# Kernel tuning notes

Hardware: AMD Instinct MI355X
Metric: run time of the kernel (lower is better)

Reference implementation:

```python
import jax, jax.numpy as jnp
import numpy as np

N_NODES = 50000
N_EDGES = 800000
ND = 10      # node feature dim
ED = 10      # edge feature dim
H = 128      # hidden dim
C = 2        # num classes
BN_EPS = 1e-5


def setup_inputs() -> dict:
    key = jax.random.key(0)
    ks = jax.random.split(key, 32)

    def glorot(i, shape):
        fan_in, fan_out = shape[-2], shape[-1]
        s = np.sqrt(6.0 / (fan_in + fan_out))
        return jax.random.uniform(ks[i], shape, dtype=jnp.float32, minval=-s, maxval=s)

    inp = {
        "x": jax.random.normal(ks[0], (N_NODES, ND), dtype=jnp.float32),
        "edge_index": jax.random.randint(ks[1], (2, N_EDGES), 0, N_NODES),
        "edge_attr": jax.random.normal(ks[2], (N_EDGES, ED), dtype=jnp.float32),
        # node encoder: Linear(ND,H), ReLU, Dropout, Linear(H,H)
        "ne_w1": glorot(3, (ND, H)), "ne_b1": jnp.zeros((H,), jnp.float32),
        "ne_w2": glorot(4, (H, H)),  "ne_b2": jnp.zeros((H,), jnp.float32),
        # edge encoder: Linear(ED,H), ReLU, Dropout, Linear(H,H)
        "ee_w1": glorot(5, (ED, H)), "ee_b1": jnp.zeros((H,), jnp.float32),
        "ee_w2": glorot(6, (H, H)),  "ee_b2": jnp.zeros((H,), jnp.float32),
        # edge attention: Linear(2H+ED,H), ReLU, Linear(H,1), Sigmoid
        "ea_w1": glorot(7, (2 * H + ED, H)), "ea_b1": jnp.zeros((H,), jnp.float32),
        "ea_w2": glorot(8, (H, 1)),          "ea_b2": jnp.zeros((1,), jnp.float32),
        # 3 GCN layers (weight + bias), 3 batchnorms, 2 skip linears
        "gcn_w": glorot(9, (3, H, H)),  "gcn_b": jnp.zeros((3, H), jnp.float32),
        "bn_g": jnp.ones((3, H), jnp.float32), "bn_b": jnp.zeros((3, H), jnp.float32),
        "skip_w": glorot(10, (2, H, H)), "skip_b": jnp.zeros((2, H), jnp.float32),
        # classifier: Linear(2H,H), ReLU, Linear(H,H//2), ReLU, Linear(H//2,C)
        "cl_w1": glorot(11, (2 * H, H)),   "cl_b1": jnp.zeros((H,), jnp.float32),
        "cl_w2": glorot(12, (H, H // 2)),  "cl_b2": jnp.zeros((H // 2,), jnp.float32),
        "cl_w3": glorot(13, (H // 2, C)),  "cl_b3": jnp.zeros((C,), jnp.float32),
    }
    return inp


def reference(x, edge_index, edge_attr,
              ne_w1, ne_b1, ne_w2, ne_b2,
              ee_w1, ee_b1, ee_w2, ee_b2,
              ea_w1, ea_b1, ea_w2, ea_b2,
              gcn_w, gcn_b, bn_g, bn_b, skip_w, skip_b,
              cl_w1, cl_b1, cl_w2, cl_b2, cl_w3, cl_b3):
    n = x.shape[0]
    row, col = edge_index[0], edge_index[1]

    # node encoder (dropout is identity in eval)
    h = jax.nn.relu(x @ ne_w1 + ne_b1) @ ne_w2 + ne_b2

    # GCN normalization with self-loops (PyG GCNConv, symmetric norm)
    sl = jnp.arange(n)
    row_f = jnp.concatenate([row, sl])   # source
    col_f = jnp.concatenate([col, sl])   # target
    deg = jax.ops.segment_sum(jnp.ones_like(row_f, dtype=h.dtype), col_f, num_segments=n)
    dinv = jnp.where(deg > 0, jax.lax.rsqrt(jnp.maximum(deg, 1.0)) * (deg > 0), 0.0)
    dinv = jnp.where(deg > 0, deg ** -0.5, 0.0)
    norm = (dinv[row_f] * dinv[col_f])[:, None]  # [E+N, 1]

    for i in range(3):
        h_prev = h
        m = h @ gcn_w[i]                                            # transform
        h = jax.ops.segment_sum(norm * m[row_f], col_f, num_segments=n) + gcn_b[i]
        # batchnorm (batch statistics over nodes)
        mu = h.mean(axis=0)
        var = h.var(axis=0)
        h = (h - mu) / jnp.sqrt(var + BN_EPS) * bn_g[i] + bn_b[i]
        h = jax.nn.relu(h)
        if i > 0:
            h = h + h_prev @ skip_w[i - 1] + skip_b[i - 1]

    # edge-level head
    h_r = h[row]            # [E, H]
    h_c = h[col]            # [E, H]
    edge_repr = jnp.concatenate([h_r, h_c], axis=1)                 # [E, 2H]
    edge_feat = jax.nn.relu(edge_attr @ ee_w1 + ee_b1) @ ee_w2 + ee_b2
    att_in = jnp.concatenate([h_r, h_c, edge_attr], axis=1)         # [E, 2H+ED]
    att = jax.nn.sigmoid(jax.nn.relu(att_in @ ea_w1 + ea_b1) @ ea_w2 + ea_b2)  # [E,1]
    w_ef = att * edge_feat
    edge_repr = edge_repr + jnp.concatenate([w_ef, w_ef], axis=1)

    # classifier MLP
    z = jax.nn.relu(edge_repr @ cl_w1 + cl_b1)
    z = jax.nn.relu(z @ cl_w2 + cl_b2)
    logits = z @ cl_w3 + cl_b3                                       # [E, C]
    return logits
```

## Files before the change

kernel.cpp:

```cpp
#include <hip/hip_runtime.h>
#include <math.h>

#define NN 50000
#define NE 800000
#define H 128

typedef short bf16x8 __attribute__((ext_vector_type(8)));
typedef unsigned short u16x8 __attribute__((ext_vector_type(8)));
typedef float f32x4 __attribute__((ext_vector_type(4)));
typedef unsigned short u16;

__device__ inline u16 f2b(float f) {
  unsigned u = __float_as_uint(f);
  return (u16)((u + 0x7FFF + ((u >> 16) & 1)) >> 16);
}
__device__ inline float b2f(u16 s) { return __uint_as_float(((unsigned)s) << 16); }

__global__ void k_prep(const float* __restrict__ ea_w1, const float* __restrict__ cl_w1,
                       const float* __restrict__ ee_w2, const float* __restrict__ cl_w2,
                       const float* __restrict__ gcn_w, const float* __restrict__ skip_w,
                       const float* __restrict__ ne_w2, const float* __restrict__ ee_w1,
                       u16* __restrict__ WP) {
  int idx = blockIdx.x * 256 + threadIdx.x;
  if (idx >= 212992) return;
  float v;
  if (idx < 16384) {
    int n = idx >> 7, k = idx & 127;
    v = ne_w2[k * 128 + n];
  } else if (idx < 65536) {
    int lo = idx - 16384; int i = lo >> 14; int n = (lo >> 7) & 127, k = lo & 127;
    v = gcn_w[i * 16384 + k * 128 + n];
  } else if (idx < 98304) {
    int lo = idx - 65536; int i = lo >> 14; int n = (lo >> 7) & 127, k = lo & 127;
    v = skip_w[i * 16384 + k * 128 + n];
  } else if (idx < 163840) {
    int lo = idx - 98304; int tab = lo >> 14; int n = (lo >> 7) & 127, k = lo & 127;
    if (tab == 0) v = ea_w1[k * 128 + n];
    else if (tab == 1) v = cl_w1[k * 128 + n];
    else if (tab == 2) v = ea_w1[(128 + k) * 128 + n];
    else v = cl_w1[(128 + k) * 128 + n];
  } else if (idx < 180224) {
    int lo = idx - 163840; int n = lo >> 7, k = lo & 127;
    v = cl_w1[k * 128 + n] + cl_w1[(128 + k) * 128 + n];
  } else if (idx < 196608) {
    int lo = idx - 180224; int n = lo >> 7, k = lo & 127;
    v = ee_w2[k * 128 + n];
  } else if (idx < 204800) {
    int lo = idx - 196608; int n = lo >> 7, k = lo & 127;
    v = cl_w2[k * 64 + n];
  } else if (idx < 208896) {
    int lo = idx - 204800; int n = lo >> 5, k = lo & 31;
    v = (k < 10) ? ee_w1[k * 128 + n] : 0.f;
  } else {
    int lo = idx - 208896; int n = lo >> 5, k = lo & 31;
    v = (k < 10) ? ea_w1[(256 + k) * 128 + n] : 0.f;
  }
  WP[idx] = f2b(v);
}

__global__ __launch_bounds__(256) void k_rowenc(
    const float* __restrict__ x, const float* __restrict__ w1,
    const float* __restrict__ b1, u16* __restrict__ t1) {
  __shared__ float xs[16][10];
  int t = threadIdx.x;
  int base = blockIdx.x * 16;
  for (int idx = t; idx < 160; idx += 256) xs[idx / 10][idx % 10] = x[base * 10 + idx];
  __syncthreads();
  int j = t & 127, eg = t >> 7;
  float acc[8];
#pragma unroll
  for (int i = 0; i < 8; ++i) acc[i] = b1[j];
  for (int k = 0; k < 10; ++k) {
    float w = w1[k * H + j];
#pragma unroll
    for (int i = 0; i < 8; ++i) acc[i] += xs[eg * 8 + i][k] * w;
  }
#pragma unroll
  for (int i = 0; i < 8; ++i) t1[(long)(base + eg * 8 + i) * H + j] = f2b(fmaxf(acc[i], 0.f));
}


__global__ __launch_bounds__(256, 2) void k_ngemm(
    const u16* __restrict__ A, const u16* __restrict__ WT,
    const float* __restrict__ bias, u16* __restrict__ outB) {
  __shared__ u16 As[128 * 128];
  int t = threadIdx.x;
  long base = (long)blockIdx.x * 128;
  for (int idx = t; idx < 128 * 16; idx += 256) {
    int row = idx >> 4, k8 = (idx & 15) * 8;
    long gr = base + row; if (gr >= NN) gr = 0;
    uint4 v = *(const uint4*)(A + gr * 128 + k8);
    *(uint4*)(As + row * 128 + (k8 ^ ((row & 7) * 8))) = v;
  }
  __syncthreads();
  int l = t & 63, w = t >> 6;
  int wrow = w * 32;
  int cl_ = l & 15, gr = l >> 4, ko = gr * 8;
  f32x4 acc[2][8];
#pragma unroll
  for (int nt = 0; nt < 8; ++nt) {
    float bb = bias[nt * 16 + cl_];
#pragma unroll
    for (int mt = 0; mt < 2; ++mt) { acc[mt][nt][0] = bb; acc[mt][nt][1] = bb; acc[mt][nt][2] = bb; acc[mt][nt][3] = bb; }
  }
#pragma unroll
  for (int c = 0; c < 4; ++c) {
    bf16x8 a[2], b[8];
#pragma unroll
    for (int mt = 0; mt < 2; ++mt) {
      int row = wrow + mt * 16 + cl_;
      a[mt] = *(const bf16x8*)(As + row * 128 + ((c * 32 + ko) ^ ((row & 7) * 8)));
    }
#pragma unroll
    for (int nt = 0; nt < 8; ++nt)
      b[nt] = *(const bf16x8*)(WT + (nt * 16 + cl_) * 128 + c * 32 + ko);
#pragma unroll
    for (int mt = 0; mt < 2; ++mt)
#pragma unroll
      for (int nt = 0; nt < 8; ++nt)
        acc[mt][nt] = __builtin_amdgcn_mfma_f32_16x16x32_bf16(a[mt], b[nt], acc[mt][nt], 0, 0, 0);
  }
#pragma unroll
  for (int mt = 0; mt < 2; ++mt)
#pragma unroll
    for (int r = 0; r < 4; ++r) {
      long row = base + wrow + mt * 16 + gr * 4 + r;
      if (row >= NN) continue;
#pragma unroll
      for (int nt = 0; nt < 8; ++nt)
        outB[row * 128 + nt * 16 + cl_] = f2b(acc[mt][nt][r]);
    }
}

__global__ __launch_bounds__(256, 2) void k_gcnskip(
    const u16* __restrict__ Ain, const u16* __restrict__ WTg, const u16* __restrict__ WTs,
    const float* __restrict__ dinv, u16* __restrict__ mn, float* __restrict__ Af) {
  __shared__ u16 As[128 * 128];
  int t = threadIdx.x;
  long base = (long)blockIdx.x * 128;
  for (int idx = t; idx < 128 * 16; idx += 256) {
    int row = idx >> 4, k8 = (idx & 15) * 8;
    long gr = base + row; if (gr >= NN) gr = 0;
    uint4 v = *(const uint4*)(Ain + gr * 128 + k8);
    *(uint4*)(As + row * 128 + (k8 ^ ((row & 7) * 8))) = v;
  }
  __syncthreads();
  const u16* WT = blockIdx.y ? WTs : WTg;
  int l = t & 63, w = t >> 6;
  int wrow = w * 32;
  int cl_ = l & 15, gr = l >> 4, ko = gr * 8;
  f32x4 acc[2][8];
#pragma unroll
  for (int nt = 0; nt < 8; ++nt)
#pragma unroll
    for (int mt = 0; mt < 2; ++mt) { acc[mt][nt][0] = 0.f; acc[mt][nt][1] = 0.f; acc[mt][nt][2] = 0.f; acc[mt][nt][3] = 0.f; }
#pragma unroll
  for (int c = 0; c < 4; ++c) {
    bf16x8 a[2], b[8];
#pragma unroll
    for (int mt = 0; mt < 2; ++mt) {
      int row = wrow + mt * 16 + cl_;
      a[mt] = *(const bf16x8*)(As + row * 128 + ((c * 32 + ko) ^ ((row & 7) * 8)));
    }
#pragma unroll
    for (int nt = 0; nt < 8; ++nt)
      b[nt] = *(const bf16x8*)(WT + (nt * 16 + cl_) * 128 + c * 32 + ko);
#pragma unroll
    for (int mt = 0; mt < 2; ++mt)
#pragma unroll
      for (int nt = 0; nt < 8; ++nt)
        acc[mt][nt] = __builtin_amdgcn_mfma_f32_16x16x32_bf16(a[mt], b[nt], acc[mt][nt], 0, 0, 0);
  }
  bool isG = (blockIdx.y == 0);
#pragma unroll
  for (int mt = 0; mt < 2; ++mt)
#pragma unroll
    for (int r = 0; r < 4; ++r) {
      long row = base + wrow + mt * 16 + gr * 4 + r;
      if (row >= NN) continue;
      float dv = isG ? dinv[row] : 0.f;
#pragma unroll
      for (int nt = 0; nt < 8; ++nt) {
        int col = nt * 16 + cl_;
        if (isG) mn[row * 128 + col] = f2b(dv * acc[mt][nt][r]);
        else Af[row * 128 + col] = acc[mt][nt][r];
      }
    }
}

__global__ __launch_bounds__(256, 2) void k_ntab(
    const u16* __restrict__ A, const u16* __restrict__ WPt4,
    const float* __restrict__ ea_b1, const float* __restrict__ cl_b1,
    u16* __restrict__ T1, u16* __restrict__ T2) {
  __shared__ u16 As[128 * 128];
  int t = threadIdx.x;
  long base = (long)blockIdx.x * 128;
  for (int idx = t; idx < 128 * 16; idx += 256) {
    int row = idx >> 4, k8 = (idx & 15) * 8;
    long gr = base + row; if (gr >= NN) gr = 0;
    uint4 v = *(const uint4*)(A + gr * 128 + k8);
    *(uint4*)(As + row * 128 + (k8 ^ ((row & 7) * 8))) = v;
  }
  __syncthreads();
  int y = blockIdx.y;
  const u16* WT = WPt4 + y * 16384;
  const float* bias = (y == 0) ? ea_b1 : ((y == 1) ? cl_b1 : nullptr);
  u16* outT = (y < 2) ? T1 : T2;
  int colOff = (y & 1) * 128;
  int l = t & 63, w = t >> 6;
  int wrow = w * 32;
  int cl_ = l & 15, gr = l >> 4, ko = gr * 8;
  f32x4 acc[2][8];
#pragma unroll
  for (int nt = 0; nt < 8; ++nt) {
    float bb = bias ? bias[nt * 16 + cl_] : 0.f;
#pragma unroll
    for (int mt = 0; mt < 2; ++mt) { acc[mt][nt][0] = bb; acc[mt][nt][1] = bb; acc[mt][nt][2] = bb; acc[mt][nt][3] = bb; }
  }
#pragma unroll
  for (int c = 0; c < 4; ++c) {
    bf16x8 a[2], b[8];
#pragma unroll
    for (int mt = 0; mt < 2; ++mt) {
      int row = wrow + mt * 16 + cl_;
      a[mt] = *(const bf16x8*)(As + row * 128 + ((c * 32 + ko) ^ ((row & 7) * 8)));
    }
#pragma unroll
    for (int nt = 0; nt < 8; ++nt)
      b[nt] = *(const bf16x8*)(WT + (nt * 16 + cl_) * 128 + c * 32 + ko);
#pragma unroll
    for (int mt = 0; mt < 2; ++mt)
#pragma unroll
      for (int nt = 0; nt < 8; ++nt)
        acc[mt][nt] = __builtin_amdgcn_mfma_f32_16x16x32_bf16(a[mt], b[nt], acc[mt][nt], 0, 0, 0);
  }
#pragma unroll
  for (int mt = 0; mt < 2; ++mt)
#pragma unroll
    for (int r = 0; r < 4; ++r) {
      long row = base + wrow + mt * 16 + gr * 4 + r;
      if (row >= NN) continue;
#pragma unroll
      for (int nt = 0; nt < 8; ++nt)
        outT[row * 256 + colOff + nt * 16 + cl_] = f2b(acc[mt][nt][r]);
    }
}

__global__ void k_deg(const int* __restrict__ col, unsigned* __restrict__ deg) {
  int e = blockIdx.x * 256 + threadIdx.x;
  if (e < NE) atomicAdd(&deg[col[e]], 1u);
}

__global__ __launch_bounds__(256) void k_scan1(const unsigned* __restrict__ deg,
                                               int* __restrict__ bsum) {
  __shared__ int s[256];
  int t = threadIdx.x, v = blockIdx.x * 256 + t;
  s[t] = (v < NN) ? (int)deg[v] : 0;
  __syncthreads();
  for (int off = 128; off > 0; off >>= 1) {
    if (t < off) s[t] += s[t + off];
    __syncthreads();
  }
  if (t == 0) bsum[blockIdx.x] = s[0];
}
__global__ __launch_bounds__(256) void k_scan2(const int* __restrict__ bsum,
                                               int* __restrict__ boff, int nb) {
  __shared__ int s[256];
  int t = threadIdx.x;
  int v = (t < nb) ? bsum[t] : 0;
  s[t] = v;
  __syncthreads();
  for (int off = 1; off < 256; off <<= 1) {
    int x = (t >= off) ? s[t - off] : 0;
    __syncthreads();
    s[t] += x;
    __syncthreads();
  }
  if (t < nb) boff[t] = s[t] - v;
}
__global__ __launch_bounds__(256) void k_scan3(const unsigned* __restrict__ deg,
                                               const int* __restrict__ boff,
                                               int* __restrict__ offs, int* __restrict__ cursor,
                                               float* __restrict__ dinv) {
  __shared__ int s[256];
  int t = threadIdx.x, v = blockIdx.x * 256 + t;
  int d = (v < NN) ? (int)deg[v] : 0;
  s[t] = d;
  __syncthreads();
  for (int off = 1; off < 256; off <<= 1) {
    int x = (t >= off) ? s[t - off] : 0;
    __syncthreads();
    s[t] += x;
    __syncthreads();
  }
  int excl = s[t] - d + boff[blockIdx.x];
  if (v < NN) {
    offs[v] = excl; cursor[v] = excl;
    dinv[v] = 1.0f / sqrtf((float)(d + 1));
  }
}
__global__ void k_fill(const int* __restrict__ ei, int* __restrict__ cursor,
                       int* __restrict__ elr, int* __restrict__ ecn, int* __restrict__ eid) {
  int e = blockIdx.x * 256 + threadIdx.x;
  if (e < NE) {
    int c = ei[NE + e];
    int pos = atomicAdd(&cursor[c], 1);
    elr[pos] = ei[e];
    ecn[pos] = c;
    eid[pos] = e;
  }
}

__global__ __launch_bounds__(256) void k_agg(
    const int* __restrict__ offs, const unsigned* __restrict__ deg,
    const int* __restrict__ elr, const float* __restrict__ dinv,
    const u16* __restrict__ mn, const float* __restrict__ gb,
    float* __restrict__ agg, double* __restrict__ sums) {
  __shared__ float s_lds[16][128];
  __shared__ float q_lds[16][128];
  int t = threadIdx.x;
  int slot = t >> 4;
  int j8 = (t & 15) * 8;
  float ps[8], pq[8];
#pragma unroll
  for (int k = 0; k < 8; ++k) { ps[k] = 0.f; pq[k] = 0.f; }
  int vbase = blockIdx.x * 64;
  for (int nn = 0; nn < 4; ++nn) {
    int v = vbase + nn * 16 + slot;
    if (v < NN) {
      float acc[8];
      u16x8 m0 = *(const u16x8*)(mn + (long)v * 128 + j8);
#pragma unroll
      for (int k = 0; k < 8; ++k) acc[k] = b2f(m0[k]);
      int start = offs[v];
      int cnt = (int)deg[v];
      for (int i = 0; i < cnt; ++i) {
        u16x8 m = *(const u16x8*)(mn + (long)elr[start + i] * 128 + j8);
#pragma unroll
        for (int k = 0; k < 8; ++k) acc[k] += b2f(m[k]);
      }
      float dv = dinv[v];
#pragma unroll
      for (int k = 0; k < 8; ++k) {
        acc[k] = dv * acc[k] + gb[j8 + k];
        ps[k] += acc[k];
        pq[k] += acc[k] * acc[k];
      }
      *(float4*)(agg + (long)v * 128 + j8) = make_float4(acc[0], acc[1], acc[2], acc[3]);
      *(float4*)(agg + (long)v * 128 + j8 + 4) = make_float4(acc[4], acc[5], acc[6], acc[7]);
    }
  }
#pragma unroll
  for (int k = 0; k < 8; ++k) { s_lds[slot][j8 + k] = ps[k]; q_lds[slot][j8 + k] = pq[k]; }
  __syncthreads();
  if (t < 128) {
    float s = 0.f;
#pragma unroll
    for (int sl = 0; sl < 16; ++sl) s += s_lds[sl][t];
    atomicAdd(&sums[t], (double)s);
  } else {
    int j = t - 128;
    float q = 0.f;
#pragma unroll
    for (int sl = 0; sl < 16; ++sl) q += q_lds[sl][j];
    atomicAdd(&sums[128 + j], (double)q);
  }
}

template <bool SKIP>
__global__ __launch_bounds__(256) void k_bnskip(
    const float* __restrict__ agg, const double* __restrict__ sums,
    const float* __restrict__ g, const float* __restrict__ b,
    const float* __restrict__ skipv, const float* __restrict__ skipb,
    u16* __restrict__ hb) {
  int idx = blockIdx.x * 256 + threadIdx.x;
  int j = idx & 127;
  double mu = sums[j] * (1.0 / NN);
  double var = sums[128 + j] * (1.0 / NN) - mu * mu;
  float inv = (float)(1.0 / sqrt(var + 1e-5));
  float val = (float)((double)agg[idx] - mu) * inv * g[j] + b[j];
  val = fmaxf(val, 0.f);
  if (SKIP) val += skipv[idx] + skipb[j];
  hb[idx] = f2b(val);
}

#define EPB 128
__global__ __launch_bounds__(256, 2) void k_edge(
    const int* __restrict__ elr, const int* __restrict__ ecn, const int* __restrict__ eid,
    const float* __restrict__ eaf,
    const u16* __restrict__ T1, const u16* __restrict__ T2,
    const float* __restrict__ ee_b1, const float* __restrict__ ee_b2,
    const float* __restrict__ ea_w2, const float* __restrict__ ea_b2,
    const u16* __restrict__ WT_ee1, const u16* __restrict__ WT_eae,
    const u16* __restrict__ WT_ee2, const u16* __restrict__ WT_ab,
    const u16* __restrict__ WT_cl2,
    const float* __restrict__ cl_b2, const float* __restrict__ cl_w3,
    const float* __restrict__ cl_b3,
    float* __restrict__ out) {
  __shared__ u16 ebuf[128 * 128];
  __shared__ u16 ustage[8192];
  __shared__ float attP[256];
  __shared__ float attS[128];

  int t = threadIdx.x;
  long ebase = (long)blockIdx.x * EPB;
  int e = t & 127, half = t >> 7;
  int jb0 = half * 64;
  int rn = elr[ebase + e];
  int cn = ecn[ebase + e];

  int l = t & 63, w = t >> 6;
  int wrow = w * 32;
  int cl_ = l & 15, g4 = l >> 4, ko = g4 * 8;

  int srow = wrow + (l >> 1);
  int cq = (l & 1) * 32;
  int rs = elr[ebase + srow];
  int cs = ecn[ebase + srow];
  u16* cstage = ustage + w * 2048;

  u16x8 h1p[8];
#pragma unroll
  for (int k = 0; k < 8; ++k)
    h1p[k] = *(const u16x8*)(T1 + (long)rn * 256 + jb0 + k * 8);
  u16x8 v1p[8];
#pragma unroll
  for (int k = 0; k < 8; ++k) {
    int hh = k >> 2, kk = k & 3;
    v1p[k] = *(const u16x8*)(T1 + (long)rs * 256 + 128 + hh * 64 + cq + kk * 8);
  }

  {
    int k0 = half * 16;
    long ge = eid[ebase + e];
    const float* src = eaf + ge * 10;
#pragma unroll
    for (int k = 0; k < 16; ++k) {
      int kk = k0 + k;
      ustage[e * 32 + kk] = (kk < 10) ? f2b(src[kk]) : (u16)0;
    }
  }
  __syncthreads();

  {
    bf16x8 aEA[2];
#pragma unroll
    for (int mt = 0; mt < 2; ++mt)
      aEA[mt] = *(const bf16x8*)(ustage + (wrow + mt * 16 + cl_) * 32 + ko);
    bf16x8 b[8];
#pragma unroll
    for (int nt = 0; nt < 8; ++nt)
      b[nt] = *(const bf16x8*)(WT_eae + (nt * 16 + cl_) * 32 + ko);
#pragma unroll
    for (int mt = 0; mt < 2; ++mt)
#pragma unroll
      for (int nt = 0; nt < 8; ++nt) {
        f32x4 pa = {0.f, 0.f, 0.f, 0.f};
        pa = __builtin_amdgcn_mfma_f32_16x16x32_bf16(aEA[mt], b[nt], pa, 0, 0, 0);
#pragma unroll
        for (int r = 0; r < 4; ++r) {
          int row = wrow + mt * 16 + g4 * 4 + r;
          int col = nt * 16 + cl_;
          ebuf[row * 128 + (col ^ ((row & 7) * 8))] = f2b(pa[r]);
        }
      }
  }
  __syncthreads();

  {
    float s = 0.f;
#pragma unroll
    for (int k = 0; k < 8; ++k) {
      int jb = jb0 + k * 8;
      u16x8 h1 = h1p[k];
      u16x8 h2 = *(const u16x8*)(T2 + (long)cn * 256 + jb);
      u16x8 pp = *(const u16x8*)(ebuf + e * 128 + (jb ^ ((e & 7) * 8)));
#pragma unroll
      for (int i = 0; i < 8; ++i)
        s += fmaxf(b2f(h1[i]) + b2f(h2[i]) + b2f(pp[i]), 0.f) * ea_w2[jb + i];
    }
    attP[half * 128 + e] = s;
  }
  __syncthreads();

  if (t < 128) attS[t] = 1.f / (1.f + __expf(-(attP[t] + attP[128 + t] + ea_b2[0])));

  {
    bf16x8 aEA[2];
#pragma unroll
    for (int mt = 0; mt < 2; ++mt)
      aEA[mt] = *(const bf16x8*)(ustage + (wrow + mt * 16 + cl_) * 32 + ko);
    bf16x8 b[8];
#pragma unroll
    for (int nt = 0; nt < 8; ++nt)
      b[nt] = *(const bf16x8*)(WT_ee1 + (nt * 16 + cl_) * 32 + ko);
#pragma unroll
    for (int mt = 0; mt < 2; ++mt)
#pragma unroll
      for (int nt = 0; nt < 8; ++nt) {
        float bb = ee_b1[nt * 16 + cl_];
        f32x4 ua;
        ua[0] = bb; ua[1] = bb; ua[2] = bb; ua[3] = bb;
        ua = __builtin_amdgcn_mfma_f32_16x16x32_bf16(aEA[mt], b[nt], ua, 0, 0, 0);
#pragma unroll
        for (int r = 0; r < 4; ++r) {
          int row = wrow + mt * 16 + g4 * 4 + r;
          int col = nt * 16 + cl_;
          ebuf[row * 128 + (col ^ ((row & 7) * 8))] = f2b(fmaxf(ua[r], 0.f));
        }
      }
  }
  __syncthreads();

  {
    bf16x8 a2[4][2];
#pragma unroll
    for (int c = 0; c < 4; ++c)
#pragma unroll
      for (int mt = 0; mt < 2; ++mt) {
        int row = wrow + mt * 16 + cl_;
        a2[c][mt] = *(const bf16x8*)(ebuf + row * 128 + ((c * 32 + ko) ^ ((row & 7) * 8)));
      }
#pragma unroll
    for (int hh = 0; hh < 2; ++hh) {
      f32x4 acc[2][4];
#pragma unroll
      for (int n4 = 0; n4 < 4; ++n4) {
        float bb = ee_b2[(hh * 4 + n4) * 16 + cl_];
#pragma unroll
        for (int mt = 0; mt < 2; ++mt) { acc[mt][n4][0] = bb; acc[mt][n4][1] = bb; acc[mt][n4][2] = bb; acc[mt][n4][3] = bb; }
      }
#pragma unroll
      for (int c = 0; c < 4; ++c)
#pragma unroll
        for (int n4 = 0; n4 < 4; ++n4) {
          bf16x8 b = *(const bf16x8*)(WT_ee2 + ((hh * 4 + n4) * 16 + cl_) * 128 + c * 32 + ko);
#pragma unroll
          for (int mt = 0; mt < 2; ++mt)
            acc[mt][n4] = __builtin_amdgcn_mfma_f32_16x16x32_bf16(a2[c][mt], b, acc[mt][n4], 0, 0, 0);
        }
#pragma unroll
      for (int mt = 0; mt < 2; ++mt)
#pragma unroll
        for (int r = 0; r < 4; ++r) {
          int row = wrow + mt * 16 + g4 * 4 + r;
          float av = attS[row];
#pragma unroll
          for (int n4 = 0; n4 < 4; ++n4) {
            int col = (hh * 4 + n4) * 16 + cl_;
            ebuf[row * 128 + (col ^ ((row & 7) * 8))] = f2b(av * acc[mt][n4][r]);
          }
        }
    }
  }

  {
    bf16x8 a2[4][2];
#pragma unroll
    for (int c = 0; c < 4; ++c)
#pragma unroll
      for (int mt = 0; mt < 2; ++mt) {
        int row = wrow + mt * 16 + cl_;
        a2[c][mt] = *(const bf16x8*)(ebuf + row * 128 + ((c * 32 + ko) ^ ((row & 7) * 8)));
      }
#pragma unroll
    for (int hh = 0; hh < 2; ++hh) {
      f32x4 acc[2][4];
#pragma unroll
      for (int n4 = 0; n4 < 4; ++n4)
#pragma unroll
        for (int mt = 0; mt < 2; ++mt) { acc[mt][n4][0] = 0.f; acc[mt][n4][1] = 0.f; acc[mt][n4][2] = 0.f; acc[mt][n4][3] = 0.f; }
#pragma unroll
      for (int c = 0; c < 4; ++c)
#pragma unroll
        for (int n4 = 0; n4 < 4; ++n4) {
          bf16x8 b = *(const bf16x8*)(WT_ab + ((hh * 4 + n4) * 16 + cl_) * 128 + c * 32 + ko);
#pragma unroll
          for (int mt = 0; mt < 2; ++mt)
            acc[mt][n4] = __builtin_amdgcn_mfma_f32_16x16x32_bf16(a2[c][mt], b, acc[mt][n4], 0, 0, 0);
        }
      u16x8 v2[4];
#pragma unroll
      for (int k = 0; k < 4; ++k)
        v2[k] = *(const u16x8*)(T2 + (long)cs * 256 + 128 + hh * 64 + cq + k * 8);
#pragma unroll
      for (int k = 0; k < 4; ++k) {
        u16x8 p;
#pragma unroll
        for (int i = 0; i < 8; ++i) p[i] = f2b(b2f(v1p[hh * 4 + k][i]) + b2f(v2[k][i]));
        *(u16x8*)(cstage + (srow & 31) * 64 + ((cq + k * 8) ^ ((srow & 7) * 8))) = p;
      }
#pragma unroll
      for (int mt = 0; mt < 2; ++mt)
#pragma unroll
        for (int r = 0; r < 4; ++r) {
          int row = wrow + mt * 16 + g4 * 4 + r;
#pragma unroll
          for (int n4 = 0; n4 < 4; ++n4) {
            int col = (hh * 4 + n4) * 16 + cl_;
            int cc = col - hh * 64;
            float v = acc[mt][n4][r] + b2f(cstage[(row & 31) * 64 + (cc ^ ((row & 7) * 8))]);
            ebuf[row * 128 + (col ^ ((row & 7) * 8))] = f2b(fmaxf(v, 0.f));
          }
        }
    }
  }

  f32x4 acc2[2][4];
#pragma unroll
  for (int nt = 0; nt < 4; ++nt) {
    float bb = cl_b2[nt * 16 + cl_];
#pragma unroll
    for (int mt = 0; mt < 2; ++mt) { acc2[mt][nt][0] = bb; acc2[mt][nt][1] = bb; acc2[mt][nt][2] = bb; acc2[mt][nt][3] = bb; }
  }
#pragma unroll
  for (int c = 0; c < 4; ++c) {
    bf16x8 a[2], b[4];
#pragma unroll
    for (int mt = 0; mt < 2; ++mt) {
      int row = wrow + mt * 16 + cl_;
      a[mt] = *(const bf16x8*)(ebuf + row * 128 + ((c * 32 + ko) ^ ((row & 7) * 8)));
    }
#pragma unroll
    for (int nt = 0; nt < 4; ++nt)
      b[nt] = *(const bf16x8*)(WT_cl2 + (nt * 16 + cl_) * 128 + c * 32 + ko);
#pragma unroll
    for (int mt = 0; mt < 2; ++mt)
#pragma unroll
      for (int nt = 0; nt < 4; ++nt)
        acc2[mt][nt] = __builtin_amdgcn_mfma_f32_16x16x32_bf16(a[mt], b[nt], acc2[mt][nt], 0, 0, 0);
  }
#pragma unroll
  for (int mt = 0; mt < 2; ++mt)
#pragma unroll
    for (int r = 0; r < 4; ++r) {
      int row = wrow + mt * 16 + g4 * 4 + r;
#pragma unroll
      for (int nt = 0; nt < 4; ++nt) {
        int col = nt * 16 + cl_;
        ebuf[row * 128 + (col ^ ((row & 7) * 8))] = f2b(fmaxf(acc2[mt][nt][r], 0.f));
      }
    }
  __syncthreads();

  if (t < 128) {
    long ge = eid[ebase + t];
    float o0 = cl_b3[0], o1 = cl_b3[1];
    for (int k8 = 0; k8 < 64; k8 += 8) {
      u16x8 v = *(const u16x8*)(ebuf + t * 128 + (k8 ^ ((t & 7) * 8)));
#pragma unroll
      for (int i = 0; i < 8; ++i) {
        float z = b2f(v[i]);
        o0 += z * cl_w3[(k8 + i) * 2];
        o1 += z * cl_w3[(k8 + i) * 2 + 1];
      }
    }
    *(float2*)(out + ge * 2) = make_float2(o0, o1);
  }
}

extern "C" void kernel_launch(void* const* d_in, const int* in_sizes, int n_in,
                              void* d_out, int out_size, void* d_ws, size_t ws_size,
                              hipStream_t stream) {
  (void)in_sizes; (void)n_in; (void)out_size; (void)ws_size;
  const float* x = (const float*)d_in[0];
  const int* ei = (const int*)d_in[1];
  const float* eattr = (const float*)d_in[2];
  const float* ne_w1 = (const float*)d_in[3];
  const float* ne_b1 = (const float*)d_in[4];
  const float* ne_w2 = (const float*)d_in[5];
  const float* ne_b2 = (const float*)d_in[6];
  const float* ee_w1 = (const float*)d_in[7];
  const float* ee_b1 = (const float*)d_in[8];
  const float* ee_w2 = (const float*)d_in[9];
  const float* ee_b2 = (const float*)d_in[10];
  const float* ea_w1 = (const float*)d_in[11];
  const float* ea_b1 = (const float*)d_in[12];
  const float* ea_w2 = (const float*)d_in[13];
  const float* ea_b2 = (const float*)d_in[14];
  const float* gcn_w = (const float*)d_in[15];
  const float* gcn_b = (const float*)d_in[16];
  const float* bn_g = (const float*)d_in[17];
  const float* bn_b = (const float*)d_in[18];
  const float* skip_w = (const float*)d_in[19];
  const float* skip_b = (const float*)d_in[20];
  const float* cl_w1 = (const float*)d_in[21];
  const float* cl_b1 = (const float*)d_in[22];
  const float* cl_w2 = (const float*)d_in[23];
  const float* cl_b2 = (const float*)d_in[24];
  const float* cl_w3 = (const float*)d_in[25];
  const float* cl_b3 = (const float*)d_in[26];
  float* out = (float*)d_out;

  char* ws = (char*)d_ws;
  u16* hb0 = (u16*)ws;
  u16* hb1 = (u16*)(ws + 12800000);
  float* A = (float*)(ws + 25600000);
  u16* mn = (u16*)(ws + 51200000);
  float* agg = (float*)(ws + 64000000);
  unsigned* deg = (unsigned*)(ws + 89600000);
  float* dinv = (float*)(ws + 89800000);
  double* sums = (double*)(ws + 90000000);
  u16* WP = (u16*)(ws + 90002048);
  int* offs = (int*)(ws + 90428032);
  int* cursor = (int*)(ws + 90628032);
  int* bsum = (int*)(ws + 90828032);
  int* boff = (int*)(ws + 90829056);
  int* elr = (int*)(ws + 90830080);
  int* ecn = (int*)(ws + 94030080);
  int* eid = (int*)(ws + 97230080);
  u16* T1 = (u16*)A;
  u16* T2 = (u16*)agg;

  u16* WP_ne2 = WP;
  u16* WP_gcn = WP + 16384;
  u16* WP_skip = WP + 65536;
  u16* WP_t4 = WP + 98304;
  u16* WP_ab = WP + 163840;
  u16* WP_ee2 = WP + 180224;
  u16* WP_cl2 = WP + 196608;
  u16* WP_ee1 = WP + 204800;
  u16* WP_eae = WP + 208896;

  const int* col = ei + NE;
  const int NGB = (NN + 255) / 256;
  const int NGB128 = (NN + 127) / 128;

  k_prep<<<832, 256, 0, stream>>>(ea_w1, cl_w1, ee_w2, cl_w2, gcn_w, skip_w, ne_w2, ee_w1, WP);
  hipMemsetAsync(deg, 0, NN * sizeof(unsigned), stream);
  k_deg<<<(NE + 255) / 256, 256, 0, stream>>>(col, deg);
  k_scan1<<<NGB, 256, 0, stream>>>(deg, bsum);
  k_scan2<<<1, 256, 0, stream>>>(bsum, boff, NGB);
  k_scan3<<<NGB, 256, 0, stream>>>(deg, boff, offs, cursor, dinv);
  k_fill<<<(NE + 255) / 256, 256, 0, stream>>>(ei, cursor, elr, ecn, eid);

  k_rowenc<<<NN / 16, 256, 0, stream>>>(x, ne_w1, ne_b1, hb1);
  k_ngemm<<<NGB128, 256, 0, stream>>>(hb1, WP_ne2, ne_b2, hb0);

  u16* hin = hb0; u16* hout = hb1;
  for (int i = 0; i < 3; ++i) {
    if (i > 0)
      k_gcnskip<<<dim3(NGB128, 2), 256, 0, stream>>>(hin, WP_gcn + (long)i * 16384,
                                                     WP_skip + (long)(i - 1) * 16384, dinv, mn, A);
    else
      k_gcnskip<<<dim3(NGB128, 1), 256, 0, stream>>>(hin, WP_gcn, nullptr, dinv, mn, nullptr);
    hipMemsetAsync(sums, 0, 256 * sizeof(double), stream);
    k_agg<<<(NN + 63) / 64, 256, 0, stream>>>(offs, deg, elr, dinv, mn, gcn_b + i * H, agg, sums);
    if (i > 0)
      k_bnskip<true><<<NN * H / 256, 256, 0, stream>>>(
          agg, sums, bn_g + i * H, bn_b + i * H, A, skip_b + (i - 1) * H, hout);
    else
      k_bnskip<false><<<NN * H / 256, 256, 0, stream>>>(
          agg, sums, bn_g, bn_b, nullptr, nullptr, hout);
    u16* tmp = hin; hin = hout; hout = tmp;
  }

  k_ntab<<<dim3(NGB128, 4), 256, 0, stream>>>(hin, WP_t4, ea_b1, cl_b1, T1, T2);

  k_edge<<<NE / EPB, 256, 0, stream>>>(
      elr, ecn, eid, eattr, T1, T2, ee_b1, ee_b2, ea_w2, ea_b2,
      WP_ee1, WP_eae, WP_ee2, WP_ab, WP_cl2, cl_b2, cl_w3, cl_b3, out);
}
```

Baseline: 907.1 us.

## Fuse node encoder, merge per-node GEMM grids, defer edge table loads

Replaces the scalar first node-encoder layer and the separate second-layer GEMM with one kernel that does both layers on MFMA. The intermediate activation stays in shared memory and x is converted to padded bf16. The GCN/skip and node-table kernels now loop over their weight matrices within one block instead of using blockIdx.y, so the A tile is loaded from global once rather than per y-slice. The edge kernel no longer prefetches T1 rows into registers at the start, and loads them later where they are used. This should cut register pressure, but the loads are no longer hidden behind other work.

```diff
diff --git a/kernel.cpp b/kernel.cpp
--- a/kernel.cpp
+++ b/kernel.cpp
@@ -20,9 +20,9 @@
                        const float* __restrict__ ee_w2, const float* __restrict__ cl_w2,
                        const float* __restrict__ gcn_w, const float* __restrict__ skip_w,
                        const float* __restrict__ ne_w2, const float* __restrict__ ee_w1,
-                       u16* __restrict__ WP) {
+                       const float* __restrict__ ne_w1, u16* __restrict__ WP) {
   int idx = blockIdx.x * 256 + threadIdx.x;
-  if (idx >= 212992) return;
+  if (idx >= 217088) return;
   float v;
   if (idx < 16384) {
     int n = idx >> 7, k = idx & 127;
@@ -51,55 +51,61 @@
   } else if (idx < 208896) {
     int lo = idx - 204800; int n = lo >> 5, k = lo & 31;
     v = (k < 10) ? ee_w1[k * 128 + n] : 0.f;
-  } else {
+  } else if (idx < 212992) {
     int lo = idx - 208896; int n = lo >> 5, k = lo & 31;
     v = (k < 10) ? ea_w1[(256 + k) * 128 + n] : 0.f;
+  } else {
+    int lo = idx - 212992; int n = lo >> 5, k = lo & 31;
+    v = (k < 10) ? ne_w1[k * 128 + n] : 0.f;
   }
   WP[idx] = f2b(v);
 }
 
-__global__ __launch_bounds__(256) void k_rowenc(
-    const float* __restrict__ x, const float* __restrict__ w1,
-    const float* __restrict__ b1, u16* __restrict__ t1) {
-  __shared__ float xs[16][10];
-  int t = threadIdx.x;
-  int base = blockIdx.x * 16;
-  for (int idx = t; idx < 160; idx += 256) xs[idx / 10][idx % 10] = x[base * 10 + idx];
-  __syncthreads();
-  int j = t & 127, eg = t >> 7;
-  float acc[8];
-#pragma unroll
-  for (int i = 0; i < 8; ++i) acc[i] = b1[j];
-  for (int k = 0; k < 10; ++k) {
-    float w = w1[k * H + j];
-#pragma unroll
-    for (int i = 0; i < 8; ++i) acc[i] += xs[eg * 8 + i][k] * w;
-  }
-#pragma unroll
-  for (int i = 0; i < 8; ++i) t1[(long)(base + eg * 8 + i) * H + j] = f2b(fmaxf(acc[i], 0.f));
-}
-
-
-__global__ __launch_bounds__(256, 2) void k_ngemm(
-    const u16* __restrict__ A, const u16* __restrict__ WT,
-    const float* __restrict__ bias, u16* __restrict__ outB) {
+__global__ __launch_bounds__(256, 2) void k_nodeenc(
+    const float* __restrict__ x, const u16* __restrict__ WT1,
+    const u16* __restrict__ WT2, const float* __restrict__ b1,
+    const float* __restrict__ b2, u16* __restrict__ outB) {
+  __shared__ u16 XL[128 * 32];
   __shared__ u16 As[128 * 128];
   int t = threadIdx.x;
   long base = (long)blockIdx.x * 128;
-  for (int idx = t; idx < 128 * 16; idx += 256) {
-    int row = idx >> 4, k8 = (idx & 15) * 8;
+  for (int idx = t; idx < 128 * 32; idx += 256) {
+    int row = idx >> 5, kk = idx & 31;
     long gr = base + row; if (gr >= NN) gr = 0;
-    uint4 v = *(const uint4*)(A + gr * 128 + k8);
-    *(uint4*)(As + row * 128 + (k8 ^ ((row & 7) * 8))) = v;
+    XL[idx] = (kk < 10) ? f2b(x[gr * 10 + kk]) : (u16)0;
   }
   __syncthreads();
   int l = t & 63, w = t >> 6;
   int wrow = w * 32;
-  int cl_ = l & 15, gr = l >> 4, ko = gr * 8;
+  int cl_ = l & 15, g4 = l >> 4, ko = g4 * 8;
+  {
+    bf16x8 a[2], b[8];
+#pragma unroll
+    for (int mt = 0; mt < 2; ++mt)
+      a[mt] = *(const bf16x8*)(XL + (wrow + mt * 16 + cl_) * 32 + ko);
+#pragma unroll
+    for (int nt = 0; nt < 8; ++nt)
+      b[nt] = *(const bf16x8*)(WT1 + (nt * 16 + cl_) * 32 + ko);
+#pragma unroll
+    for (int mt = 0; mt < 2; ++mt)
+#pragma unroll
+      for (int nt = 0; nt < 8; ++nt) {
+        float bb = b1[nt * 16 + cl_];
+        f32x4 ua;
+        ua[0] = bb; ua[1] = bb; ua[2] = bb; ua[3] = bb;
+        ua = __builtin_amdgcn_mfma_f32_16x16x32_bf16(a[mt], b[nt], ua, 0, 0, 0);
+#pragma unroll
+        for (int r = 0; r < 4; ++r) {
+          int row = wrow + mt * 16 + g4 * 4 + r;
+          int col = nt * 16 + cl_;
+          As[row * 128 + (col ^ ((row & 7) * 8))] = f2b(fmaxf(ua[r], 0.f));
+        }
+      }
+  }
   f32x4 acc[2][8];
 #pragma unroll
   for (int nt = 0; nt < 8; ++nt) {
-    float bb = bias[nt * 16 + cl_];
+    float bb = b2[nt * 16 + cl_];
 #pragma unroll
     for (int mt = 0; mt < 2; ++mt) { acc[mt][nt][0] = bb; acc[mt][nt][1] = bb; acc[mt][nt][2] = bb; acc[mt][nt][3] = bb; }
   }
@@ -113,7 +119,7 @@
     }
 #pragma unroll
     for (int nt = 0; nt < 8; ++nt)
-      b[nt] = *(const bf16x8*)(WT + (nt * 16 + cl_) * 128 + c * 32 + ko);
+      b[nt] = *(const bf16x8*)(WT2 + (nt * 16 + cl_) * 128 + c * 32 + ko);
 #pragma unroll
     for (int mt = 0; mt < 2; ++mt)
 #pragma unroll
@@ -124,7 +130,7 @@
   for (int mt = 0; mt < 2; ++mt)
 #pragma unroll
     for (int r = 0; r < 4; ++r) {
-      long row = base + wrow + mt * 16 + gr * 4 + r;
+      long row = base + wrow + mt * 16 + g4 * 4 + r;
       if (row >= NN) continue;
 #pragma unroll
       for (int nt = 0; nt < 8; ++nt)
@@ -145,47 +151,78 @@
     *(uint4*)(As + row * 128 + (k8 ^ ((row & 7) * 8))) = v;
   }
   __syncthreads();
-  const u16* WT = blockIdx.y ? WTs : WTg;
   int l = t & 63, w = t >> 6;
   int wrow = w * 32;
-  int cl_ = l & 15, gr = l >> 4, ko = gr * 8;
-  f32x4 acc[2][8];
-#pragma unroll
-  for (int nt = 0; nt < 8; ++nt)
-#pragma unroll
-    for (int mt = 0; mt < 2; ++mt) { acc[mt][nt][0] = 0.f; acc[mt][nt][1] = 0.f; acc[mt][nt][2] = 0.f; acc[mt][nt][3] = 0.f; }
-#pragma unroll
-  for (int c = 0; c < 4; ++c) {
-    bf16x8 a[2], b[8];
-#pragma unroll
-    for (int mt = 0; mt < 2; ++mt) {
-      int row = wrow + mt * 16 + cl_;
-      a[mt] = *(const bf16x8*)(As + row * 128 + ((c * 32 + ko) ^ ((row & 7) * 8)));
-    }
+  int cl_ = l & 15, g4 = l >> 4, ko = g4 * 8;
+  {
+    f32x4 acc[2][8];
 #pragma unroll
     for (int nt = 0; nt < 8; ++nt)
-      b[nt] = *(const bf16x8*)(WT + (nt * 16 + cl_) * 128 + c * 32 + ko);
-#pragma unroll
-    for (int mt = 0; mt < 2; ++mt)
+#pragma unroll
+      for (int mt = 0; mt < 2; ++mt) { acc[mt][nt][0] = 0.f; acc[mt][nt][1] = 0.f; acc[mt][nt][2] = 0.f; acc[mt][nt][3] = 0.f; }
+#pragma unroll
+    for (int c = 0; c < 4; ++c) {
+      bf16x8 a[2], b[8];
+#pragma unroll
+      for (int mt = 0; mt < 2; ++mt) {
+        int row = wrow + mt * 16 + cl_;
+        a[mt] = *(const bf16x8*)(As + row * 128 + ((c * 32 + ko) ^ ((row & 7) * 8)));
+      }
 #pragma unroll
       for (int nt = 0; nt < 8; ++nt)
-        acc[mt][nt] = __builtin_amdgcn_mfma_f32_16x16x32_bf16(a[mt], b[nt], acc[mt][nt], 0, 0, 0);
-  }
-  bool isG = (blockIdx.y == 0);
-#pragma unroll
-  for (int mt = 0; mt < 2; ++mt)
-#pragma unroll
-    for (int r = 0; r < 4; ++r) {
-      long row = base + wrow + mt * 16 + gr * 4 + r;
-      if (row >= NN) continue;
-      float dv = isG ? dinv[row] : 0.f;
-#pragma unroll
-      for (int nt = 0; nt < 8; ++nt) {
-        int col = nt * 16 + cl_;
-        if (isG) mn[row * 128 + col] = f2b(dv * acc[mt][nt][r]);
-        else Af[row * 128 + col] = acc[mt][nt][r];
-      }
-    }
+        b[nt] = *(const bf16x8*)(WTg + (nt * 16 + cl_) * 128 + c * 32 + ko);
+#pragma unroll
+      for (int mt = 0; mt < 2; ++mt)
+#pragma unroll
+        for (int nt = 0; nt < 8; ++nt)
+          acc[mt][nt] = __builtin_amdgcn_mfma_f32_16x16x32_bf16(a[mt], b[nt], acc[mt][nt], 0, 0, 0);
+    }
+#pragma unroll
+    for (int mt = 0; mt < 2; ++mt)
+#pragma unroll
+      for (int r = 0; r < 4; ++r) {
+        long row = base + wrow + mt * 16 + g4 * 4 + r;
+        if (row >= NN) continue;
+        float dv = dinv[row];
+#pragma unroll
+        for (int nt = 0; nt < 8; ++nt)
+          mn[row * 128 + nt * 16 + cl_] = f2b(dv * acc[mt][nt][r]);
+      }
+  }
+  if (WTs) {
+    f32x4 acc[2][8];
+#pragma unroll
+    for (int nt = 0; nt < 8; ++nt)
+#pragma unroll
+      for (int mt = 0; mt < 2; ++mt) { acc[mt][nt][0] = 0.f; acc[mt][nt][1] = 0.f; acc[mt][nt][2] = 0.f; acc[mt][nt][3] = 0.f; }
+#pragma unroll
+    for (int c = 0; c < 4; ++c) {
+      bf16x8 a[2], b[8];
+#pragma unroll
+      for (int mt = 0; mt < 2; ++mt) {
+        int row = wrow + mt * 16 + cl_;
+        a[mt] = *(const bf16x8*)(As + row * 128 + ((c * 32 + ko) ^ ((row & 7) * 8)));
+      }
+#pragma unroll
+      for (int nt = 0; nt < 8; ++nt)
+        b[nt] = *(const bf16x8*)(WTs + (nt * 16 + cl_) * 128 + c * 32 + ko);
+#pragma unroll
+      for (int mt = 0; mt < 2; ++mt)
+#pragma unroll
+        for (int nt = 0; nt < 8; ++nt)
+          acc[mt][nt] = __builtin_amdgcn_mfma_f32_16x16x32_bf16(a[mt], b[nt], acc[mt][nt], 0, 0, 0);
+    }
+#pragma unroll
+    for (int mt = 0; mt < 2; ++mt)
+#pragma unroll
+      for (int r = 0; r < 4; ++r) {
+        long row = base + wrow + mt * 16 + g4 * 4 + r;
+        if (row >= NN) continue;
+#pragma unroll
+        for (int nt = 0; nt < 8; ++nt)
+          Af[row * 128 + nt * 16 + cl_] = acc[mt][nt][r];
+      }
+  }
 }
 
 __global__ __launch_bounds__(256, 2) void k_ntab(
@@ -202,48 +239,49 @@
     *(uint4*)(As + row * 128 + (k8 ^ ((row & 7) * 8))) = v;
   }
   __syncthreads();
-  int y = blockIdx.y;
-  const u16* WT = WPt4 + y * 16384;
-  const float* bias = (y == 0) ? ea_b1 : ((y == 1) ? cl_b1 : nullptr);
-  u16* outT = (y < 2) ? T1 : T2;
-  int colOff = (y & 1) * 128;
   int l = t & 63, w = t >> 6;
   int wrow = w * 32;
-  int cl_ = l & 15, gr = l >> 4, ko = gr * 8;
-  f32x4 acc[2][8];
-#pragma unroll
-  for (int nt = 0; nt < 8; ++nt) {
-    float bb = bias ? bias[nt * 16 + cl_] : 0.f;
-#pragma unroll
-    for (int mt = 0; mt < 2; ++mt) { acc[mt][nt][0] = bb; acc[mt][nt][1] = bb; acc[mt][nt][2] = bb; acc[mt][nt][3] = bb; }
-  }
-#pragma unroll
-  for (int c = 0; c < 4; ++c) {
-    bf16x8 a[2], b[8];
-#pragma unroll
-    for (int mt = 0; mt < 2; ++mt) {
-      int row = wrow + mt * 16 + cl_;
-      a[mt] = *(const bf16x8*)(As + row * 128 + ((c * 32 + ko) ^ ((row & 7) * 8)));
-    }
-#pragma unroll
-    for (int nt = 0; nt < 8; ++nt)
-      b[nt] = *(const bf16x8*)(WT + (nt * 16 + cl_) * 128 + c * 32 + ko);
-#pragma unroll
-    for (int mt = 0; mt < 2; ++mt)
+  int cl_ = l & 15, g4 = l >> 4, ko = g4 * 8;
+  for (int y = 0; y < 4; ++y) {
+    const u16* WT = WPt4 + y * 16384;
+    const float* bias = (y == 0) ? ea_b1 : ((y == 1) ? cl_b1 : nullptr);
+    u16* outT = (y < 2) ? T1 : T2;
+    int colOff = (y & 1) * 128;
+    f32x4 acc[2][8];
+#pragma unroll
+    for (int nt = 0; nt < 8; ++nt) {
+      float bb = bias ? bias[nt * 16 + cl_] : 0.f;
+#pragma unroll
+      for (int mt = 0; mt < 2; ++mt) { acc[mt][nt][0] = bb; acc[mt][nt][1] = bb; acc[mt][nt][2] = bb; acc[mt][nt][3] = bb; }
+    }
+#pragma unroll
+    for (int c = 0; c < 4; ++c) {
+      bf16x8 a[2], b[8];
+#pragma unroll
+      for (int mt = 0; mt < 2; ++mt) {
+        int row = wrow + mt * 16 + cl_;
+        a[mt] = *(const bf16x8*)(As + row * 128 + ((c * 32 + ko) ^ ((row & 7) * 8)));
+      }
 #pragma unroll
       for (int nt = 0; nt < 8; ++nt)
-        acc[mt][nt] = __builtin_amdgcn_mfma_f32_16x16x32_bf16(a[mt], b[nt], acc[mt][nt], 0, 0, 0);
-  }
-#pragma unroll
-  for (int mt = 0; mt < 2; ++mt)
-#pragma unroll
-    for (int r = 0; r < 4; ++r) {
-      long row = base + wrow + mt * 16 + gr * 4 + r;
-      if (row >= NN) continue;
-#pragma unroll
-      for (int nt = 0; nt < 8; ++nt)
-        outT[row * 256 + colOff + nt * 16 + cl_] = f2b(acc[mt][nt][r]);
-    }
+        b[nt] = *(const bf16x8*)(WT + (nt * 16 + cl_) * 128 + c * 32 + ko);
+#pragma unroll
+      for (int mt = 0; mt < 2; ++mt)
+#pragma unroll
+        for (int nt = 0; nt < 8; ++nt)
+          acc[mt][nt] = __builtin_amdgcn_mfma_f32_16x16x32_bf16(a[mt], b[nt], acc[mt][nt], 0, 0, 0);
+    }
+#pragma unroll
+    for (int mt = 0; mt < 2; ++mt)
+#pragma unroll
+      for (int r = 0; r < 4; ++r) {
+        long row = base + wrow + mt * 16 + g4 * 4 + r;
+        if (row >= NN) continue;
+#pragma unroll
+        for (int nt = 0; nt < 8; ++nt)
+          outT[row * 256 + colOff + nt * 16 + cl_] = f2b(acc[mt][nt][r]);
+      }
+  }
 }
 
 __global__ void k_deg(const int* __restrict__ col, unsigned* __restrict__ deg) {
@@ -419,17 +457,6 @@
   int cs = ecn[ebase + srow];
   u16* cstage = ustage + w * 2048;
 
-  u16x8 h1p[8];
-#pragma unroll
-  for (int k = 0; k < 8; ++k)
-    h1p[k] = *(const u16x8*)(T1 + (long)rn * 256 + jb0 + k * 8);
-  u16x8 v1p[8];
-#pragma unroll
-  for (int k = 0; k < 8; ++k) {
-    int hh = k >> 2, kk = k & 3;
-    v1p[k] = *(const u16x8*)(T1 + (long)rs * 256 + 128 + hh * 64 + cq + kk * 8);
-  }
-
   {
     int k0 = half * 16;
     long ge = eid[ebase + e];
@@ -469,10 +496,8 @@
 
   {
     float s = 0.f;
-#pragma unroll
-    for (int k = 0; k < 8; ++k) {
-      int jb = jb0 + k * 8;
-      u16x8 h1 = h1p[k];
+    for (int jb = jb0; jb < jb0 + 64; jb += 8) {
+      u16x8 h1 = *(const u16x8*)(T1 + (long)rn * 256 + jb);
       u16x8 h2 = *(const u16x8*)(T2 + (long)cn * 256 + jb);
       u16x8 pp = *(const u16x8*)(ebuf + e * 128 + (jb ^ ((e & 7) * 8)));
 #pragma unroll
@@ -579,15 +604,17 @@
           for (int mt = 0; mt < 2; ++mt)
             acc[mt][n4] = __builtin_amdgcn_mfma_f32_16x16x32_bf16(a2[c][mt], b, acc[mt][n4], 0, 0, 0);
         }
-      u16x8 v2[4];
-#pragma unroll
-      for (int k = 0; k < 4; ++k)
+      u16x8 v1[4], v2[4];
+#pragma unroll
+      for (int k = 0; k < 4; ++k) {
+        v1[k] = *(const u16x8*)(T1 + (long)rs * 256 + 128 + hh * 64 + cq + k * 8);
         v2[k] = *(const u16x8*)(T2 + (long)cs * 256 + 128 + hh * 64 + cq + k * 8);
+      }
 #pragma unroll
       for (int k = 0; k < 4; ++k) {
         u16x8 p;
 #pragma unroll
-        for (int i = 0; i < 8; ++i) p[i] = f2b(b2f(v1p[hh * 4 + k][i]) + b2f(v2[k][i]));
+        for (int i = 0; i < 8; ++i) p[i] = f2b(b2f(v1[k][i]) + b2f(v2[k][i]));
         *(u16x8*)(cstage + (srow & 31) * 64 + ((cq + k * 8) ^ ((srow & 7) * 8))) = p;
       }
 #pragma unroll
@@ -702,13 +729,13 @@
   float* dinv = (float*)(ws + 89800000);
   double* sums = (double*)(ws + 90000000);
   u16* WP = (u16*)(ws + 90002048);
-  int* offs = (int*)(ws + 90428032);
-  int* cursor = (int*)(ws + 90628032);
-  int* bsum = (int*)(ws + 90828032);
-  int* boff = (int*)(ws + 90829056);
-  int* elr = (int*)(ws + 90830080);
-  int* ecn = (int*)(ws + 94030080);
-  int* eid = (int*)(ws + 97230080);
+  int* offs = (int*)(ws + 90436224);
+  int* cursor = (int*)(ws + 90636224);
+  int* bsum = (int*)(ws + 90836224);
+  int* boff = (int*)(ws + 90837248);
+  int* elr = (int*)(ws + 90838272);
+  int* ecn = (int*)(ws + 94038272);
+  int* eid = (int*)(ws + 97238272);
   u16* T1 = (u16*)A;
   u16* T2 = (u16*)agg;
 
@@ -721,12 +748,13 @@
   u16* WP_cl2 = WP + 196608;
   u16* WP_ee1 = WP + 204800;
   u16* WP_eae = WP + 208896;
+  u16* WP_ne1 = WP + 212992;
 
   const int* col = ei + NE;
   const int NGB = (NN + 255) / 256;
   const int NGB128 = (NN + 127) / 128;
 
-  k_prep<<<832, 256, 0, stream>>>(ea_w1, cl_w1, ee_w2, cl_w2, gcn_w, skip_w, ne_w2, ee_w1, WP);
+  k_prep<<<848, 256, 0, stream>>>(ea_w1, cl_w1, ee_w2, cl_w2, gcn_w, skip_w, ne_w2, ee_w1, ne_w1, WP);
   hipMemsetAsync(deg, 0, NN * sizeof(unsigned), stream);
   k_deg<<<(NE + 255) / 256, 256, 0, stream>>>(col, deg);
   k_scan1<<<NGB, 256, 0, stream>>>(deg, bsum);
@@ -734,16 +762,13 @@
   k_scan3<<<NGB, 256, 0, stream>>>(deg, boff, offs, cursor, dinv);
   k_fill<<<(NE + 255) / 256, 256, 0, stream>>>(ei, cursor, elr, ecn, eid);
 
-  k_rowenc<<<NN / 16, 256, 0, stream>>>(x, ne_w1, ne_b1, hb1);
-  k_ngemm<<<NGB128, 256, 0, stream>>>(hb1, WP_ne2, ne_b2, hb0);
+  k_nodeenc<<<NGB128, 256, 0, stream>>>(x, WP_ne1, WP_ne2, ne_b1, ne_b2, hb0);
 
   u16* hin = hb0; u16* hout = hb1;
   for (int i = 0; i < 3; ++i) {
-    if (i > 0)
-      k_gcnskip<<<dim3(NGB128, 2), 256, 0, stream>>>(hin, WP_gcn + (long)i * 16384,
-                                                     WP_skip + (long)(i - 1) * 16384, dinv, mn, A);
-    else
-      k_gcnskip<<<dim3(NGB128, 1), 256, 0, stream>>>(hin, WP_gcn, nullptr, dinv, mn, nullptr);
+    k_gcnskip<<<NGB128, 256, 0, stream>>>(hin, WP_gcn + (long)i * 16384,
+                                          (i > 0) ? (WP_skip + (long)(i - 1) * 16384) : nullptr,
+                                          dinv, mn, A);
     hipMemsetAsync(sums, 0, 256 * sizeof(double), stream);
     k_agg<<<(NN + 63) / 64, 256, 0, stream>>>(offs, deg, elr, dinv, mn, gcn_b + i * H, agg, sums);
     if (i > 0)
@@ -755,7 +780,7 @@
     u16* tmp = hin; hin = hout; hout = tmp;
   }
 
-  k_ntab<<<dim3(NGB128, 4), 256, 0, stream>>>(hin, WP_t4, ea_b1, cl_b1, T1, T2);
+  k_ntab<<<NGB128, 256, 0, stream>>>(hin, WP_t4, ea_b1, cl_b1, T1, T2);
 
   k_edge<<<NE / EPB, 256, 0, stream>>>(
       elr, ecn, eid, eattr, T1, T2, ee_b1, ee_b2, ea_w2, ea_b2,
```

New measurement: 884.2 us. 1.03x faster.
